# Optimization experiments

Measured on AMD Instinct MI355X. Metric: run time of the kernel, lower is better.

Reference implementation:

```python
import jax, jax.numpy as jnp
import numpy as np
from jax import lax

B = 1
D, H, W = 16, 16, 32
L = D * H * W
C = 96          # hidden_dim
DIN = 96        # d_inner = expansion_factor(1) * hidden_dim
N = 16          # d_state
R = 6           # dt_rank = ceil(C / 16)
K = 8           # scan directions: 4 axis orders x {fwd, bwd}
PERMS = [(0, 1, 2), (1, 2, 0), (2, 0, 1), (2, 1, 0)]


def _ln(x, w, b, eps):
    m = x.mean(-1, keepdims=True)
    v = ((x - m) ** 2).mean(-1, keepdims=True)
    return (x - m) * lax.rsqrt(v + eps) * w + b


def _conv3d(x, w, b, groups=1):
    y = lax.conv_general_dilated(x, w, (1, 1, 1), 'SAME', feature_group_count=groups,
                                 dimension_numbers=('NCDHW', 'OIDHW', 'NCDHW'))
    return y + b[None, :, None, None, None]


def _ss3d(x5, in_proj_w, conv_w, conv_b, x_proj_w, dt_w, dt_b, A_logs, Ds,
          out_norm_w, out_norm_b, out_proj_w):
    b, d, h, w, _ = x5.shape
    l = d * h * w
    spatial = (d, h, w)
    xz = jnp.einsum('bdhwc,ec->bdhwe', x5, in_proj_w)          # (b,d,h,w,2*DIN)
    x, z = jnp.split(xz, 2, axis=-1)
    x = jnp.transpose(x, (0, 4, 1, 2, 3))                       # (b,DIN,d,h,w)
    x = jax.nn.silu(_conv3d(x, conv_w, conv_b, groups=DIN))     # depthwise conv
    # build K/2 axis-order scans, then add reversed copies -> K directions
    xs = jnp.stack([jnp.transpose(x, (0, 1, 2 + p[0], 2 + p[1], 2 + p[2])).reshape(b, DIN, l)
                    for p in PERMS], axis=1)                    # (b,4,DIN,l)
    xs = jnp.concatenate([xs, jnp.flip(xs, -1)], axis=1)        # (b,K,DIN,l)
    x_dbl = jnp.einsum('bkdl,ked->bkel', xs, x_proj_w)          # e = R+2N
    dts, Bs, Cs = x_dbl[:, :, :R], x_dbl[:, :, R:R + N], x_dbl[:, :, R + N:]
    dts = jax.nn.softplus(jnp.einsum('bkrl,kdr->bkdl', dts, dt_w) + dt_b[None, :, :, None])
    A = -jnp.exp(A_logs)                                        # (K,DIN,N)
    # time-major for the selective scan
    dts_t = jnp.moveaxis(dts, -1, 0)                            # (l,b,K,DIN)
    xs_t = jnp.moveaxis(xs, -1, 0)
    Bs_t = jnp.moveaxis(Bs, -1, 0)                              # (l,b,K,N)
    Cs_t = jnp.moveaxis(Cs, -1, 0)

    def step(hc, inps):
        dt, u, Bt, Ct = inps
        hc = jnp.exp(dt[..., None] * A) * hc + (dt * u)[..., None] * Bt[:, :, None, :]
        y = jnp.einsum('bkdn,bkn->bkd', hc, Ct)
        return hc, y

    h0 = jnp.zeros((b, K, DIN, N), x.dtype)
    _, ys = lax.scan(step, h0, (dts_t, xs_t, Bs_t, Cs_t))       # ys: (l,b,K,DIN)
    ys = jnp.moveaxis(ys, 0, -1) + Ds[None, :, :, None] * xs    # (b,K,DIN,l)
    y_f, y_b = ys[:, :4], jnp.flip(ys[:, 4:], -1)
    acc = jnp.zeros((b, DIN, l), x.dtype)
    for i, p in enumerate(PERMS):
        inv = np.argsort(p)
        pshape = tuple(spatial[ax] for ax in p)
        for yk in (y_f[:, i], y_b[:, i]):
            yk = yk.reshape(b, DIN, *pshape)
            yk = jnp.transpose(yk, (0, 1, 2 + int(inv[0]), 2 + int(inv[1]), 2 + int(inv[2])))
            acc = acc + yk.reshape(b, DIN, l)
    y = _ln(jnp.transpose(acc, (0, 2, 1)), out_norm_w, out_norm_b, 1e-5)
    y = y.reshape(b, d, h, w, DIN) * jax.nn.silu(z)
    return jnp.einsum('bdhwe,ce->bdhwc', y, out_proj_w)


def _cab(x, cab_w1, cab_b1, cab_w2, cab_b2, ca_w1, ca_b1, ca_w2, ca_b2):
    # x: (b,C,d,h,w); conv -> GELU -> conv -> channel attention
    t = jax.nn.gelu(_conv3d(x, cab_w1, cab_b1), approximate=False)
    t = _conv3d(t, cab_w2, cab_b2)
    m = t.mean(axis=(2, 3, 4))                                  # global avg pool (b,C)
    v = jax.nn.relu(m @ ca_w1.T + ca_b1)
    v = jax.nn.sigmoid(v @ ca_w2.T + ca_b2)
    return t * v[:, :, None, None, None]


def _forward(inp, ln1_w, ln1_b, skip1, skip2, ln2_w, ln2_b, in_proj_w, conv_w, conv_b,
             x_proj_w, dt_w, dt_b, A_logs, Ds, out_norm_w, out_norm_b, out_proj_w,
             cab_w1, cab_b1, cab_w2, cab_b2, ca_w1, ca_b1, ca_w2, ca_b2, x_size):
    b, l, c = inp.shape
    d, h, w = x_size
    x5 = inp.reshape(b, d, h, w, c)
    xn = _ln(x5, ln1_w, ln1_b, 1e-6)
    attn = _ss3d(xn, in_proj_w, conv_w, conv_b, x_proj_w, dt_w, dt_b, A_logs, Ds,
                 out_norm_w, out_norm_b, out_proj_w)
    x = x5 * skip1 + attn                                       # drop_path = identity (rate 0)
    y2 = jnp.transpose(_ln(x, ln2_w, ln2_b, 1e-5), (0, 4, 1, 2, 3))
    cab = _cab(y2, cab_w1, cab_b1, cab_w2, cab_b2, ca_w1, ca_b1, ca_w2, ca_b2)
    x = x * skip2 + jnp.transpose(cab, (0, 2, 3, 4, 1))
    return x.reshape(b, l, c)


def setup_inputs() -> dict:
    key = jax.random.key(0)
    ks = jax.random.split(key, 12)
    g = lambda i, shp, s=0.02: jax.random.normal(ks[i], shp, jnp.float32) * s
    return {
        'inp': jax.random.normal(ks[0], (B, L, C), jnp.float32),
        'x_size': (D, H, W),
        'ln1_w': jnp.ones((C,), jnp.float32), 'ln1_b': jnp.zeros((C,), jnp.float32),
        'skip1': jnp.ones((C,), jnp.float32), 'skip2': jnp.ones((C,), jnp.float32),
        'ln2_w': jnp.ones((C,), jnp.float32), 'ln2_b': jnp.zeros((C,), jnp.float32),
        'in_proj_w': g(1, (2 * DIN, C)),
        'conv_w': g(2, (DIN, 1, 3, 3, 3), 0.1), 'conv_b': jnp.zeros((DIN,), jnp.float32),
        'x_proj_w': g(3, (K, R + 2 * N, DIN)),
        'dt_w': g(4, (K, DIN, R), 0.1), 'dt_b': g(5, (K, DIN), 0.1),
        'A_logs': jnp.log(jnp.tile(jnp.arange(1, N + 1, dtype=jnp.float32), (K, DIN, 1))),
        'Ds': jnp.ones((K, DIN), jnp.float32),
        'out_norm_w': jnp.ones((DIN,), jnp.float32), 'out_norm_b': jnp.zeros((DIN,), jnp.float32),
        'out_proj_w': g(6, (C, DIN)),
        'cab_w1': g(7, (C // 3, C, 3, 3, 3), 0.05), 'cab_b1': jnp.zeros((C // 3,), jnp.float32),
        'cab_w2': g(8, (C, C // 3, 3, 3, 3), 0.05), 'cab_b2': jnp.zeros((C,), jnp.float32),
        'ca_w1': g(9, (C // 2, C)), 'ca_b1': jnp.zeros((C // 2,), jnp.float32),
        'ca_w2': g(10, (C, C // 2)), 'ca_b2': jnp.zeros((C,), jnp.float32),
    }


def reference(inp, ln1_w, ln1_b, skip1, skip2, ln2_w, ln2_b, in_proj_w, conv_w, conv_b,
              x_proj_w, dt_w, dt_b, A_logs, Ds, out_norm_w, out_norm_b, out_proj_w,
              cab_w1, cab_b1, cab_w2, cab_b2, ca_w1, ca_b1, ca_w2, ca_b2, x_size):
    return _forward(inp, ln1_w, ln1_b, skip1, skip2, ln2_w, ln2_b, in_proj_w, conv_w, conv_b,
                    x_proj_w, dt_w, dt_b, A_logs, Ds, out_norm_w, out_norm_b, out_proj_w,
                    cab_w1, cab_b1, cab_w2, cab_b2, ca_w1, ca_b1, ca_w2, ca_b2, x_size)
```

## Files before the change

kernel.cpp:

```cpp
#include <hip/hip_runtime.h>
#include <math.h>

#define LL 8192
#define CC 96
#define DINc 96
#define NN 16
#define RR 6
#define KK 8
#define Dd 16
#define Hh 16
#define Ww 32
#define NCH 32
#define CHL 256

__constant__ int Pc_[4][3] = {{0,1,2},{1,2,0},{2,0,1},{2,1,0}};

__device__ __forceinline__ float silu_(float x){ return x / (1.f + __expf(-x)); }

__global__ void k_ln1(const float* __restrict__ inp, const float* __restrict__ w,
                      const float* __restrict__ b, float* __restrict__ xn_cm) {
    __shared__ float tile[16][97];
    __shared__ float smean[16], srstd[16];
    int l0 = blockIdx.x * 16;
    int tid = threadIdx.x;
    #pragma unroll
    for (int r = 0; r < 6; ++r) {
        int e = r * 256 + tid;
        int lo = e / 96, c = e % 96;
        tile[lo][c] = inp[(long)(l0 + lo) * 96 + c];
    }
    __syncthreads();
    {
        int lo = tid >> 4, g = tid & 15;
        float ps = 0.f;
        #pragma unroll
        for (int j = 0; j < 6; ++j) ps += tile[lo][g * 6 + j];
        #pragma unroll
        for (int o = 1; o < 16; o <<= 1) ps += __shfl_xor(ps, o, 16);
        float m = ps * (1.f / 96.f);
        float pv = 0.f;
        #pragma unroll
        for (int j = 0; j < 6; ++j) { float dd = tile[lo][g * 6 + j] - m; pv += dd * dd; }
        #pragma unroll
        for (int o = 1; o < 16; o <<= 1) pv += __shfl_xor(pv, o, 16);
        if (g == 0) { smean[lo] = m; srstd[lo] = rsqrtf(pv * (1.f / 96.f) + 1e-6f); }
    }
    __syncthreads();
    #pragma unroll
    for (int r = 0; r < 6; ++r) {
        int e = r * 256 + tid;
        int c = e >> 4, lo = e & 15;
        xn_cm[(long)c * LL + l0 + lo] = (tile[lo][c] - smean[lo]) * srstd[lo] * w[c] + b[c];
    }
}

__global__ void k_wtrans(const float* __restrict__ inpj, const float* __restrict__ xpw,
                         const float* __restrict__ w1, const float* __restrict__ w2,
                         const float* __restrict__ opw,
                         float* __restrict__ ipT, float* __restrict__ xpT,
                         float* __restrict__ wT1, float* __restrict__ wT2,
                         float* __restrict__ opT) {
    int idx = blockIdx.x * blockDim.x + threadIdx.x;
    if (idx < 82944) {
        int oc = idx & 31; int tap = (idx >> 5) % 27; int ic = idx / (32 * 27);
        wT1[idx] = w1[(oc * 96 + ic) * 27 + tap];
    }
    if (idx < 82944) {
        int oc = idx % 96; int tap = (idx / 96) % 27; int ic = idx / (96 * 27);
        wT2[idx] = w2[(oc * 32 + ic) * 27 + tap];
    }
    if (idx < 18432) {
        int e = idx % 192; int c = idx / 192;
        ipT[idx] = inpj[e * 96 + c];
    }
    if (idx < 29184) {
        int e = idx % 38; int c = (idx / 38) % 96; int k = idx / (38 * 96);
        xpT[idx] = xpw[(k * 38 + e) * 96 + c];
    }
    if (idx < 9216) {
        int c = idx % 96; int e = idx / 96;
        opT[idx] = opw[c * 96 + e];
    }
}

__global__ void k_inproj(const float* __restrict__ xn_cm, const float* __restrict__ ipT,
                         float* __restrict__ xcm, float* __restrict__ z_rm) {
    int bx = blockIdx.x;
    int eb = bx >> 5;
    int l  = ((bx & 31) << 8) + threadIdx.x;
    int e0 = eb << 3;
    float a[8];
    #pragma unroll
    for (int j = 0; j < 8; ++j) a[j] = 0.f;
    const float* wp = ipT + e0;
    for (int c = 0; c < CC; ++c) {
        float x = xn_cm[c * LL + l];
        const float4* wv = (const float4*)(wp + c * 192);
        float4 wa = wv[0], wb = wv[1];
        a[0] += x * wa.x; a[1] += x * wa.y; a[2] += x * wa.z; a[3] += x * wa.w;
        a[4] += x * wb.x; a[5] += x * wb.y; a[6] += x * wb.z; a[7] += x * wb.w;
    }
    if (e0 < DINc) {
        float* dst = xcm + (long)e0 * LL;
        #pragma unroll
        for (int j = 0; j < 8; ++j) dst[(long)j * LL + l] = a[j];
    } else {
        float* dst = z_rm + (long)l * DINc + (e0 - DINc);
        #pragma unroll
        for (int j = 0; j < 8; ++j) dst[j] = a[j];
    }
}

__global__ void k_dwconv(const float* __restrict__ xcm, const float* __restrict__ cw,
                         const float* __restrict__ cb, float* __restrict__ xs0) {
    int bx = blockIdx.x;
    int c  = bx >> 3;
    int l4 = ((bx & 7) << 8) + threadIdx.x;
    int w0 = (l4 & 7) << 2;
    int h  = (l4 >> 3) & 15;
    int d  = l4 >> 7;
    int l  = (d * Hh + h) * Ww + w0;
    float wk[27];
    #pragma unroll
    for (int t = 0; t < 27; ++t) wk[t] = cw[c * 27 + t];
    float rmask[9]; int roff[9];
    #pragma unroll
    for (int kd = 0; kd < 3; ++kd) {
        int dd = d + kd - 1;
        bool vd = (unsigned)dd < Dd; int dc = vd ? dd : 0;
        #pragma unroll
        for (int kh = 0; kh < 3; ++kh) {
            int hh = h + kh - 1;
            bool vh = (unsigned)hh < Hh; int hcl = vh ? hh : 0;
            rmask[kd * 3 + kh] = (vd && vh) ? 1.f : 0.f;
            roff[kd * 3 + kh]  = (dc * Hh + hcl) * Ww + w0;
        }
    }
    float mleft  = (w0 > 0)  ? 1.f : 0.f;
    float mright = (w0 < 28) ? 1.f : 0.f;
    float a0 = cb[c], a1 = a0, a2 = a0, a3 = a0;
    const float* xp = xcm + (long)c * LL;
    #pragma unroll
    for (int r = 0; r < 9; ++r) {
        float rm = rmask[r];
        const float* xr = xp + roff[r];
        float4 xc = *(const float4*)xr;
        float v[6];
        v[0] = xr[-1] * (rm * mleft);
        v[1] = xc.x * rm; v[2] = xc.y * rm; v[3] = xc.z * rm; v[4] = xc.w * rm;
        v[5] = xr[4] * (rm * mright);
        #pragma unroll
        for (int t = 0; t < 3; ++t) {
            float wv = wk[r * 3 + t];
            a0 += v[t + 0] * wv;
            a1 += v[t + 1] * wv;
            a2 += v[t + 2] * wv;
            a3 += v[t + 3] * wv;
        }
    }
    *(float4*)(xs0 + (long)c * LL + l) = make_float4(silu_(a0), silu_(a1), silu_(a2), silu_(a3));
}

__global__ void k_permA(float* __restrict__ xs) {
    __shared__ float lv[8192 + 256 + 16];
    int bx = blockIdx.x;
    int k = bx / 96 + 1;
    int c = bx % 96;
    const float* src = xs + (long)c * LL;
    float* dst = xs + ((long)k * DINc + c) * LL;
    int tid = threadIdx.x;
    for (int i = tid; i < LL; i += 256)
        lv[i + (i >> 5) + (i >> 9)] = src[i];
    __syncthreads();
    int p0 = Pc_[k][0], p1 = Pc_[k][1], p2 = Pc_[k][2];
    const int sp[3] = {Dd, Hh, Ww};
    int pd1 = sp[p1], pd2 = sp[p2];
    for (int i = tid; i < LL; i += 256) {
        int i2 = i % pd2;
        int t  = i / pd2;
        int i1 = t % pd1;
        int i0 = t / pd1;
        int coord[3];
        coord[p0] = i0; coord[p1] = i1; coord[p2] = i2;
        int o = (coord[0] * Hh + coord[1]) * Ww + coord[2];
        dst[i] = lv[o + (o >> 5) + (o >> 9)];
    }
}

__global__ void k_permB(float* __restrict__ xs) {
    int idx = blockIdx.x * blockDim.x + threadIdx.x;
    if (idx >= 4 * DINc * (LL / 4)) return;
    int q = idx & (LL / 4 - 1);
    int c = (idx >> 11) % DINc;
    int k = idx / (DINc * (LL / 4));
    const float4* src = (const float4*)(xs + ((long)k * DINc + c) * LL);
    float4 s = src[LL / 4 - 1 - q];
    float4* dst = (float4*)(xs + ((long)(k + 4) * DINc + c) * LL);
    dst[q] = make_float4(s.w, s.z, s.y, s.x);
}

__global__ void k_xdbl(const float* __restrict__ xs, const float* __restrict__ xpT,
                       float* __restrict__ dtr, float* __restrict__ Bb, float* __restrict__ Cb) {
    int bx = blockIdx.x;
    int k = bx >> 6;
    int rest = bx & 63;
    int eh = rest & 1;
    int lblk = rest >> 1;
    int l = (lblk << 8) + threadIdx.x;
    int e0 = eh * 19;
    float acc[19];
    #pragma unroll
    for (int e = 0; e < 19; ++e) acc[e] = 0.f;
    const float* xb = xs + (long)k * DINc * LL + l;
    const float* wb = xpT + k * DINc * 38 + e0;
    for (int c = 0; c < DINc; ++c) {
        float x = xb[(long)c * LL];
        const float* wr = wb + c * 38;
        #pragma unroll
        for (int e = 0; e < 19; ++e) acc[e] += x * wr[e];
    }
    int lq = l >> 2, q = l & 3;
    #pragma unroll
    for (int e = 0; e < 19; ++e) {
        int ge = e0 + e;
        if (ge < RR)
            dtr[((long)k * LL + l) * 6 + ge] = acc[e];
        else if (ge < RR + NN)
            Bb[(((long)k * 2048 + lq) * 16 + (ge - RR)) * 4 + q] = acc[e];
        else
            Cb[(((long)k * 2048 + lq) * 16 + (ge - RR - NN)) * 4 + q] = acc[e];
    }
}

__device__ __forceinline__ float softplus_(float x) {
    return (x > 20.f) ? x : __logf(1.f + __expf(x));
}

__global__ __launch_bounds__(512)
void k_scanf(float* __restrict__ xs_ys, const float* __restrict__ dtr,
             const float* __restrict__ Bb, const float* __restrict__ Cb,
             const float* __restrict__ A_logs, const float* __restrict__ dt_w,
             const float* __restrict__ dt_b, const float* __restrict__ Ds) {
    __shared__ __align__(16) float sdt[LL + (LL >> 7) * 4];
    __shared__ float sAp[16][33];
    __shared__ float sBc[16][33];
    __shared__ float shs[16][33];
    int bx = blockIdx.x;
    int grp = (bx & 7) * DINc + (bx >> 3);
    int k = grp / DINc;
    int tid = threadIdx.x;
    int n = tid & 15;
    int chunk = tid >> 4;
    {
        float w0 = dt_w[grp * RR + 0], w1 = dt_w[grp * RR + 1], w2 = dt_w[grp * RR + 2];
        float w3 = dt_w[grp * RR + 3], w4 = dt_w[grp * RR + 4], w5 = dt_w[grp * RR + 5];
        float dtb = dt_b[grp];
        const float* drb = dtr + (long)k * LL * 6;
        for (int i = tid; i < LL; i += 512) {
            const float2* dp = (const float2*)(drb + (long)i * 6);
            float2 d0 = dp[0], d1 = dp[1], d2 = dp[2];
            float dtl = dtb + d0.x * w0 + d0.y * w1 + d1.x * w2 + d1.y * w3 + d2.x * w4 + d2.y * w5;
            sdt[i + ((i >> 7) << 2)] = softplus_(dtl);
        }
    }
    __syncthreads();
    float A_n = -__expf(A_logs[grp * NN + n]);
    const float4* sdt4 = (const float4*)sdt;
    int dbase = chunk * 66;
    const float4* u4 = (const float4*)(xs_ys + (long)grp * LL + chunk * CHL);
    const float4* B4 = (const float4*)Bb + ((long)k * 2048 + chunk * (CHL / 4)) * 16 + n;
    const float4* C4 = (const float4*)Cb + ((long)k * 2048 + chunk * (CHL / 4)) * 16 + n;
    {
        float hc = 0.f, dsum = 0.f;
        #pragma unroll 4
        for (int q = 0; q < CHL / 4; ++q) {
            float4 dt = sdt4[dbase + q + (q >> 5)];
            float4 uu = u4[q];
            float4 Bv = B4[q * 16];
            dsum += (dt.x + dt.y) + (dt.z + dt.w);
            hc = __expf(dt.x * A_n) * hc + (dt.x * uu.x) * Bv.x;
            hc = __expf(dt.y * A_n) * hc + (dt.y * uu.y) * Bv.y;
            hc = __expf(dt.z * A_n) * hc + (dt.z * uu.z) * Bv.z;
            hc = __expf(dt.w * A_n) * hc + (dt.w * uu.w) * Bv.w;
        }
        sAp[n][chunk] = __expf(A_n * dsum);
        sBc[n][chunk] = hc;
    }
    __syncthreads();
    if (tid < 16) {
        float h = 0.f;
        for (int c = 0; c < NCH; ++c) {
            shs[tid][c] = h;
            h = sAp[tid][c] * h + sBc[tid][c];
        }
    }
    __syncthreads();
    float Dv = Ds[grp];
    float* urow = xs_ys + (long)grp * LL + chunk * CHL;
    float hc = shs[n][chunk];
    int qsel = n >> 2, csel = n & 3;
    bool b0 = (n & 1), b1 = ((n >> 1) & 1), b2 = ((n >> 2) & 1), b3 = (n >> 3);
    for (int base = 0; base < CHL; base += 16) {
        float u_lane = 0.f;
        float p[16];
        #pragma unroll
        for (int q = 0; q < 4; ++q) {
            int qq = (base >> 2) + q;
            float4 dt = sdt4[dbase + qq + (qq >> 5)];
            float4 uu = *(const float4*)(urow + base + q * 4);
            float4 Bv = B4[qq * 16];
            float4 Cv = C4[qq * 16];
            if (q == qsel)
                u_lane = (csel == 0) ? uu.x : (csel == 1) ? uu.y : (csel == 2) ? uu.z : uu.w;
            hc = __expf(dt.x * A_n) * hc + (dt.x * uu.x) * Bv.x;  p[q*4+0] = hc * Cv.x;
            hc = __expf(dt.y * A_n) * hc + (dt.y * uu.y) * Bv.y;  p[q*4+1] = hc * Cv.y;
            hc = __expf(dt.z * A_n) * hc + (dt.z * uu.z) * Bv.z;  p[q*4+2] = hc * Cv.z;
            hc = __expf(dt.w * A_n) * hc + (dt.w * uu.w) * Bv.w;  p[q*4+3] = hc * Cv.w;
        }
        float q8[8];
        #pragma unroll
        for (int m = 0; m < 8; ++m) {
            float sel = b0 ? p[2*m] : p[2*m+1];
            float r = __shfl_xor(sel, 1, 16);
            q8[m] = (b0 ? p[2*m+1] : p[2*m]) + r;
        }
        float r4[4];
        #pragma unroll
        for (int m = 0; m < 4; ++m) {
            float sel = b1 ? q8[2*m] : q8[2*m+1];
            float r = __shfl_xor(sel, 2, 16);
            r4[m] = (b1 ? q8[2*m+1] : q8[2*m]) + r;
        }
        float t2r[2];
        #pragma unroll
        for (int m = 0; m < 2; ++m) {
            float sel = b2 ? r4[2*m] : r4[2*m+1];
            float r = __shfl_xor(sel, 4, 16);
            t2r[m] = (b2 ? r4[2*m+1] : r4[2*m]) + r;
        }
        float sel = b3 ? t2r[0] : t2r[1];
        float r = __shfl_xor(sel, 8, 16);
        float yv = (b3 ? t2r[1] : t2r[0]) + r;
        urow[base + n] = yv + Dv * u_lane;
    }
}

__global__ void k_combproj(const float* __restrict__ ys, const float* __restrict__ z_rm,
                           const float* __restrict__ w, const float* __restrict__ b,
                           const float* __restrict__ opT, const float* __restrict__ inp,
                           const float* __restrict__ skip1, float* __restrict__ xafter) {
    __shared__ float sy[4][96];
    int wave = threadIdx.x >> 6;
    int lane = threadIdx.x & 63;
    int l = blockIdx.x * 4 + wave;
    int d = l >> 9, h = (l >> 5) & 15, wd = l & 31;
    int lps[4];
    lps[0] = l;
    lps[1] = (h * 32 + wd) * 16 + d;
    lps[2] = (wd * 16 + d) * 16 + h;
    lps[3] = (wd * 16 + h) * 16 + d;
    int c0 = lane, c1 = 64 + lane;
    float a0 = 0.f, a1 = 0.f;
    #pragma unroll
    for (int i = 0; i < 4; ++i) {
        a0 += ys[((long)(i * 96) + c0) * LL + lps[i]];
        a0 += ys[((long)((4 + i) * 96) + c0) * LL + (LL - 1 - lps[i])];
    }
    if (lane < 32) {
        #pragma unroll
        for (int i = 0; i < 4; ++i) {
            a1 += ys[((long)(i * 96) + c1) * LL + lps[i]];
            a1 += ys[((long)((4 + i) * 96) + c1) * LL + (LL - 1 - lps[i])];
        }
    }
    float s = a0 + a1;
    #pragma unroll
    for (int o = 1; o < 64; o <<= 1) s += __shfl_xor(s, o, 64);
    float m = s * (1.f / 96.f);
    float d0 = a0 - m;
    float d1 = (lane < 32) ? (a1 - m) : 0.f;
    float ss = d0 * d0 + d1 * d1;
    #pragma unroll
    for (int o = 1; o < 64; o <<= 1) ss += __shfl_xor(ss, o, 64);
    float r = rsqrtf(ss * (1.f / 96.f) + 1e-5f);
    float zz = z_rm[(long)l * 96 + c0];
    sy[wave][c0] = (d0 * r * w[c0] + b[c0]) * silu_(zz);
    if (lane < 32) {
        float z1 = z_rm[(long)l * 96 + c1];
        sy[wave][c1] = (d1 * r * w[c1] + b[c1]) * silu_(z1);
    }
    __syncthreads();
    int c1g = (lane < 32) ? c1 : 0;
    float o0 = 0.f, o1 = 0.f;
    #pragma unroll 4
    for (int e = 0; e < 96; ++e) {
        float ye = sy[wave][e];
        o0 += ye * opT[e * 96 + c0];
        o1 += ye * opT[e * 96 + c1g];
    }
    xafter[(long)l * 96 + c0] = inp[(long)l * 96 + c0] * skip1[c0] + o0;
    if (lane < 32)
        xafter[(long)l * 96 + c1] = inp[(long)l * 96 + c1] * skip1[c1] + o1;
}

__global__ void k_ln2(const float* __restrict__ xafter, const float* __restrict__ w,
                      const float* __restrict__ b, float* __restrict__ y2) {
    __shared__ float tile[16][97];
    __shared__ float smean[16], srstd[16];
    int l0 = blockIdx.x * 16;
    int tid = threadIdx.x;
    #pragma unroll
    for (int r = 0; r < 6; ++r) {
        int e = r * 256 + tid;
        int lo = e / 96, c = e % 96;
        tile[lo][c] = xafter[(long)(l0 + lo) * 96 + c];
    }
    __syncthreads();
    {
        int lo = tid >> 4, g = tid & 15;
        float ps = 0.f;
        #pragma unroll
        for (int j = 0; j < 6; ++j) ps += tile[lo][g * 6 + j];
        #pragma unroll
        for (int o = 1; o < 16; o <<= 1) ps += __shfl_xor(ps, o, 16);
        float m = ps * (1.f / 96.f);
        float pv = 0.f;
        #pragma unroll
        for (int j = 0; j < 6; ++j) { float dd = tile[lo][g * 6 + j] - m; pv += dd * dd; }
        #pragma unroll
        for (int o = 1; o < 16; o <<= 1) pv += __shfl_xor(pv, o, 16);
        if (g == 0) { smean[lo] = m; srstd[lo] = rsqrtf(pv * (1.f / 96.f) + 1e-5f); }
    }
    __syncthreads();
    #pragma unroll
    for (int r = 0; r < 6; ++r) {
        int e = r * 256 + tid;
        int c = e >> 4, lo = e & 15;
        y2[(long)c * LL + l0 + lo] = (tile[lo][c] - smean[lo]) * srstd[lo] * w[c] + b[c];
    }
}

__global__ void k_conv1(const float* __restrict__ y2, const float* __restrict__ wT,
                        float* __restrict__ part) {
    int bx = blockIdx.x;
    int g  = bx >> 3;
    int ocg = g & 7;
    int isp = g >> 3;
    int l4 = ((bx & 7) << 8) + threadIdx.x;
    int w0 = (l4 & 7) << 2;
    int h  = (l4 >> 3) & 15;
    int d  = l4 >> 7;
    int l  = (d * Hh + h) * Ww + w0;
    float rmask[9]; int roff[9];
    #pragma unroll
    for (int kd = 0; kd < 3; ++kd) {
        int dd = d + kd - 1;
        bool vd = (unsigned)dd < Dd; int dc = vd ? dd : 0;
        #pragma unroll
        for (int kh = 0; kh < 3; ++kh) {
            int hh = h + kh - 1;
            bool vh = (unsigned)hh < Hh; int hcl = vh ? hh : 0;
            rmask[kd * 3 + kh] = (vd && vh) ? 1.f : 0.f;
            roff[kd * 3 + kh]  = (dc * Hh + hcl) * Ww + w0;
        }
    }
    float mleft  = (w0 > 0)  ? 1.f : 0.f;
    float mright = (w0 < 28) ? 1.f : 0.f;
    float acc[16];
    #pragma unroll
    for (int j = 0; j < 16; ++j) acc[j] = 0.f;
    for (int ic = isp * 6; ic < isp * 6 + 6; ++ic) {
        const float* xp = y2 + (long)ic * LL;
        const float* wb = wT + ic * 864 + ocg * 4;
        #pragma unroll
        for (int r = 0; r < 9; ++r) {
            float rm = rmask[r];
            const float* xr = xp + roff[r];
            float4 xc = *(const float4*)xr;
            float v[6];
            v[0] = xr[-1] * (rm * mleft);
            v[1] = xc.x * rm; v[2] = xc.y * rm; v[3] = xc.z * rm; v[4] = xc.w * rm;
            v[5] = xr[4] * (rm * mright);
            #pragma unroll
            for (int t = 0; t < 3; ++t) {
                float4 wa = *(const float4*)(wb + (r * 3 + t) * 32);
                #pragma unroll
                for (int p = 0; p < 4; ++p) {
                    float x = v[t + p];
                    acc[0  + p] += x * wa.x;  acc[4  + p] += x * wa.y;
                    acc[8  + p] += x * wa.z;  acc[12 + p] += x * wa.w;
                }
            }
        }
    }
    float* pp = part + ((long)(isp * 32 + ocg * 4)) * LL + l;
    #pragma unroll
    for (int oc = 0; oc < 4; ++oc)
        *(float4*)(pp + (long)oc * LL) = make_float4(acc[oc*4+0], acc[oc*4+1], acc[oc*4+2], acc[oc*4+3]);
}

__global__ void k_gelusum(const float* __restrict__ part, const float* __restrict__ b1,
                          float* __restrict__ t1) {
    int idx = blockIdx.x * blockDim.x + threadIdx.x;
    if (idx >= 32 * LL) return;
    int l = idx & (LL - 1);
    int oc = idx >> 13;
    float s = b1[oc];
    #pragma unroll
    for (int isp = 0; isp < 16; ++isp)
        s += part[((long)(isp * 32 + oc)) * LL + l];
    t1[oc * LL + l] = 0.5f * s * (1.f + erff(s * 0.70710678118654752f));
}

__global__ void k_conv2(const float* __restrict__ t1, const float* __restrict__ wT,
                        float* __restrict__ part) {
    int bx = blockIdx.x;
    int g  = bx >> 3;
    int ocg = g % 24;
    int isp = g / 24;
    int l4 = ((bx & 7) << 8) + threadIdx.x;
    int w0 = (l4 & 7) << 2;
    int h  = (l4 >> 3) & 15;
    int d  = l4 >> 7;
    int l  = (d * Hh + h) * Ww + w0;
    float rmask[9]; int roff[9];
    #pragma unroll
    for (int kd = 0; kd < 3; ++kd) {
        int dd = d + kd - 1;
        bool vd = (unsigned)dd < Dd; int dc = vd ? dd : 0;
        #pragma unroll
        for (int kh = 0; kh < 3; ++kh) {
            int hh = h + kh - 1;
            bool vh = (unsigned)hh < Hh; int hcl = vh ? hh : 0;
            rmask[kd * 3 + kh] = (vd && vh) ? 1.f : 0.f;
            roff[kd * 3 + kh]  = (dc * Hh + hcl) * Ww + w0;
        }
    }
    float mleft  = (w0 > 0)  ? 1.f : 0.f;
    float mright = (w0 < 28) ? 1.f : 0.f;
    float acc[16];
    #pragma unroll
    for (int j = 0; j < 16; ++j) acc[j] = 0.f;
    for (int ic = isp * 4; ic < isp * 4 + 4; ++ic) {
        const float* xp = t1 + (long)ic * LL;
        const float* wb = wT + ic * 2592 + ocg * 4;
        #pragma unroll
        for (int r = 0; r < 9; ++r) {
            float rm = rmask[r];
            const float* xr = xp + roff[r];
            float4 xc = *(const float4*)xr;
            float v[6];
            v[0] = xr[-1] * (rm * mleft);
            v[1] = xc.x * rm; v[2] = xc.y * rm; v[3] = xc.z * rm; v[4] = xc.w * rm;
            v[5] = xr[4] * (rm * mright);
            #pragma unroll
            for (int t = 0; t < 3; ++t) {
                float4 wa = *(const float4*)(wb + (r * 3 + t) * 96);
                #pragma unroll
                for (int p = 0; p < 4; ++p) {
                    float x = v[t + p];
                    acc[0  + p] += x * wa.x;  acc[4  + p] += x * wa.y;
                    acc[8  + p] += x * wa.z;  acc[12 + p] += x * wa.w;
                }
            }
        }
    }
    float* pp = part + ((long)(isp * 96 + ocg * 4)) * LL + l;
    #pragma unroll
    for (int oc = 0; oc < 4; ++oc)
        *(float4*)(pp + (long)oc * LL) = make_float4(acc[oc*4+0], acc[oc*4+1], acc[oc*4+2], acc[oc*4+3]);
}

__global__ void k_conv2sum(const float* __restrict__ part, const float* __restrict__ b2,
                           float* __restrict__ t2) {
    int idx = blockIdx.x * blockDim.x + threadIdx.x;
    if (idx >= 96 * LL) return;
    int l = idx & (LL - 1);
    int oc = idx >> 13;
    float s = b2[oc];
    #pragma unroll
    for (int isp = 0; isp < 8; ++isp)
        s += part[((long)(isp * 96 + oc)) * LL + l];
    t2[oc * LL + l] = s;
}

__global__ void k_mean(const float* __restrict__ t2, float* __restrict__ mbuf) {
    __shared__ float sm[256];
    int c = blockIdx.x;
    const float4* tp = (const float4*)(t2 + (long)c * LL);
    float a = 0.f;
    for (int q = threadIdx.x; q < LL / 4; q += 256) {
        float4 v = tp[q];
        a += (v.x + v.y) + (v.z + v.w);
    }
    sm[threadIdx.x] = a;
    __syncthreads();
    for (int o = 128; o > 0; o >>= 1) {
        if (threadIdx.x < o) sm[threadIdx.x] += sm[threadIdx.x + o];
        __syncthreads();
    }
    if (threadIdx.x == 0) mbuf[c] = sm[0] * (1.f / LL);
}

__global__ void k_mlp(const float* __restrict__ mbuf, const float* __restrict__ w1,
                      const float* __restrict__ b1, const float* __restrict__ w2,
                      const float* __restrict__ b2, float* __restrict__ v2) {
    __shared__ float v[48];
    int t = threadIdx.x;
    if (t < 48) {
        float s = b1[t];
        for (int c = 0; c < 96; ++c) s += mbuf[c] * w1[t * 96 + c];
        v[t] = fmaxf(s, 0.f);
    }
    __syncthreads();
    if (t < 96) {
        float s = b2[t];
        for (int j = 0; j < 48; ++j) s += v[j] * w2[t * 48 + j];
        v2[t] = 1.f / (1.f + __expf(-s));
    }
}

__global__ void k_final(const float* __restrict__ xafter, const float* __restrict__ skip2,
                        const float* __restrict__ t2, const float* __restrict__ v2,
                        float* __restrict__ out) {
    __shared__ float tile[96][17];
    __shared__ float sk2[96], sv2[96];
    int l0 = blockIdx.x * 16;
    int tid = threadIdx.x;
    if (tid < 96) { sk2[tid] = skip2[tid]; sv2[tid] = v2[tid]; }
    #pragma unroll
    for (int r = 0; r < 6; ++r) {
        int e = r * 256 + tid;
        int c = e >> 4, lo = e & 15;
        tile[c][lo] = t2[(long)c * LL + l0 + lo];
    }
    __syncthreads();
    #pragma unroll
    for (int r = 0; r < 6; ++r) {
        int e = r * 256 + tid;
        int lo = e / 96, c = e % 96;
        long gi = (long)(l0 + lo) * 96 + c;
        out[gi] = xafter[gi] * sk2[c] + tile[c][lo] * sv2[c];
    }
}

static const size_t OFF_XS     = 0;
static const size_t OFF_Z      = 6291456;
static const size_t OFF_XCM    = 7077888;
static const size_t OFF_XN     = 7864320;
static const size_t OFF_DTRAW  = 8650752;
static const size_t OFF_BB     = 9043968;
static const size_t OFF_CB     = 10092544;
static const size_t OFF_XAFTER = 11141120;
static const size_t OFF_Y2     = 11927552;
static const size_t OFF_T1     = 12713984;
static const size_t OFF_T2     = 12976128;
static const size_t OFF_MV     = 13762560;
static const size_t OFF_WT1    = 13762816;
static const size_t OFF_WT2    = 13845760;
static const size_t OFF_IPT    = 13928704;
static const size_t OFF_XPT    = 13947136;
static const size_t OFF_OPT    = 13976320;

extern "C" void kernel_launch(void* const* d_in, const int* in_sizes, int n_in,
                              void* d_out, int out_size, void* d_ws, size_t ws_size,
                              hipStream_t stream) {
    const float* inp    = (const float*)d_in[0];
    const float* ln1_w  = (const float*)d_in[2];
    const float* ln1_b  = (const float*)d_in[3];
    const float* skip1  = (const float*)d_in[4];
    const float* skip2  = (const float*)d_in[5];
    const float* ln2_w  = (const float*)d_in[6];
    const float* ln2_b  = (const float*)d_in[7];
    const float* inpj   = (const float*)d_in[8];
    const float* conv_w = (const float*)d_in[9];
    const float* conv_b = (const float*)d_in[10];
    const float* xpw    = (const float*)d_in[11];
    const float* dt_w   = (const float*)d_in[12];
    const float* dt_b   = (const float*)d_in[13];
    const float* A_logs = (const float*)d_in[14];
    const float* Ds     = (const float*)d_in[15];
    const float* onw    = (const float*)d_in[16];
    const float* onb    = (const float*)d_in[17];
    const float* opw    = (const float*)d_in[18];
    const float* cab_w1 = (const float*)d_in[19];
    const float* cab_b1 = (const float*)d_in[20];
    const float* cab_w2 = (const float*)d_in[21];
    const float* cab_b2 = (const float*)d_in[22];
    const float* ca_w1  = (const float*)d_in[23];
    const float* ca_b1  = (const float*)d_in[24];
    const float* ca_w2  = (const float*)d_in[25];
    const float* ca_b2  = (const float*)d_in[26];

    float* ws = (float*)d_ws;
    float* xs     = ws + OFF_XS;
    float* zbuf   = ws + OFF_Z;
    float* xcm    = ws + OFF_XCM;
    float* xn     = ws + OFF_XN;
    float* dtr    = ws + OFF_DTRAW;
    float* Bb     = ws + OFF_BB;
    float* Cb     = ws + OFF_CB;
    float* xafter = ws + OFF_XAFTER;
    float* y2     = ws + OFF_Y2;
    float* t1     = ws + OFF_T1;
    float* t2     = ws + OFF_T2;
    float* mv     = ws + OFF_MV;
    float* wT1    = ws + OFF_WT1;
    float* wT2    = ws + OFF_WT2;
    float* ipT    = ws + OFF_IPT;
    float* xpT    = ws + OFF_XPT;
    float* opT    = ws + OFF_OPT;
    float* part1  = xs;
    float* part2  = xs;

    float* out = (float*)d_out;
    #define GRID(n) dim3((unsigned)(((n) + 255) / 256)), dim3(256)

    hipLaunchKernelGGL(k_ln1,     dim3(512), dim3(256),       0, stream, inp, ln1_w, ln1_b, xn);
    hipLaunchKernelGGL(k_wtrans,  GRID(82944),                0, stream, inpj, xpw, cab_w1, cab_w2, opw, ipT, xpT, wT1, wT2, opT);
    hipLaunchKernelGGL(k_inproj,  dim3(768), dim3(256),       0, stream, xn, ipT, xcm, zbuf);
    hipLaunchKernelGGL(k_dwconv,  dim3(768), dim3(256),       0, stream, xcm, conv_w, conv_b, xs);
    hipLaunchKernelGGL(k_permA,   dim3(288), dim3(256),       0, stream, xs);
    hipLaunchKernelGGL(k_permB,   GRID(4 * DINc * (LL / 4)),  0, stream, xs);
    hipLaunchKernelGGL(k_xdbl,    dim3(512), dim3(256),       0, stream, xs, xpT, dtr, Bb, Cb);
    hipLaunchKernelGGL(k_scanf,   dim3(KK * DINc), dim3(512), 0, stream, xs, dtr, Bb, Cb, A_logs, dt_w, dt_b, Ds);
    hipLaunchKernelGGL(k_combproj,dim3(LL / 4), dim3(256),    0, stream, xs, zbuf, onw, onb, opT, inp, skip1, xafter);
    hipLaunchKernelGGL(k_ln2,     dim3(512), dim3(256),       0, stream, xafter, ln2_w, ln2_b, y2);
    hipLaunchKernelGGL(k_conv1,   dim3(1024), dim3(256),      0, stream, y2, wT1, part1);
    hipLaunchKernelGGL(k_gelusum, GRID(32 * LL),              0, stream, part1, cab_b1, t1);
    hipLaunchKernelGGL(k_conv2,   dim3(1536), dim3(256),      0, stream, t1, wT2, part2);
    hipLaunchKernelGGL(k_conv2sum,GRID(96 * LL),              0, stream, part2, cab_b2, t2);
    hipLaunchKernelGGL(k_mean,    dim3(96), dim3(256),        0, stream, t2, mv);
    hipLaunchKernelGGL(k_mlp,     dim3(1), dim3(128),         0, stream, mv, ca_w1, ca_b1, ca_w2, ca_b2, mv + 96);
    hipLaunchKernelGGL(k_final,   dim3(512), dim3(256),       0, stream, xafter, skip2, t2, mv + 96, out);
    #undef GRID
}
```

Baseline: 277.1 us.

## Fuse reversed-direction copies into producers, use exp2 in scan, vectorize partial sums

The reversed scan directions are now written directly by the depthwise conv and permute kernels, so the separate k_permB pass that re-read and re-wrote half of xs goes away. The selective scan folds log2(e) into A and calls the hardware exp2 builtin instead of __expf. The two partial-sum reduction kernels (gelusum, conv2sum) now process four elements per thread with float4 loads and stores. The extra writes in k_permA are reversed-order scalar stores, which may coalesce less well.

```diff
diff --git a/kernel.cpp b/kernel.cpp
--- a/kernel.cpp
+++ b/kernel.cpp
@@ -12,6 +12,9 @@
 #define Ww 32
 #define NCH 32
 #define CHL 256
+#define LOG2E 1.44269504088896340736f
+
+__device__ __forceinline__ float ex2_(float x) { return __builtin_amdgcn_exp2f(x); }
 
 __constant__ int Pc_[4][3] = {{0,1,2},{1,2,0},{2,0,1},{2,1,0}};
 
@@ -112,7 +115,7 @@
 }
 
 __global__ void k_dwconv(const float* __restrict__ xcm, const float* __restrict__ cw,
-                         const float* __restrict__ cb, float* __restrict__ xs0) {
+                         const float* __restrict__ cb, float* __restrict__ xs) {
     int bx = blockIdx.x;
     int c  = bx >> 3;
     int l4 = ((bx & 7) << 8) + threadIdx.x;
@@ -158,7 +161,9 @@
             a3 += v[t + 3] * wv;
         }
     }
-    *(float4*)(xs0 + (long)c * LL + l) = make_float4(silu_(a0), silu_(a1), silu_(a2), silu_(a3));
+    float s0 = silu_(a0), s1 = silu_(a1), s2 = silu_(a2), s3 = silu_(a3);
+    *(float4*)(xs + (long)c * LL + l) = make_float4(s0, s1, s2, s3);
+    *(float4*)(xs + ((long)(4 * DINc) + c) * LL + (LL - 4 - l)) = make_float4(s3, s2, s1, s0);
 }
 
 __global__ void k_permA(float* __restrict__ xs) {
@@ -167,7 +172,8 @@
     int k = bx / 96 + 1;
     int c = bx % 96;
     const float* src = xs + (long)c * LL;
-    float* dst = xs + ((long)k * DINc + c) * LL;
+    float* dst  = xs + ((long)k * DINc + c) * LL;
+    float* dst4 = xs + ((long)(k + 4) * DINc + c) * LL;
     int tid = threadIdx.x;
     for (int i = tid; i < LL; i += 256)
         lv[i + (i >> 5) + (i >> 9)] = src[i];
@@ -183,20 +189,10 @@
         int coord[3];
         coord[p0] = i0; coord[p1] = i1; coord[p2] = i2;
         int o = (coord[0] * Hh + coord[1]) * Ww + coord[2];
-        dst[i] = lv[o + (o >> 5) + (o >> 9)];
-    }
-}
-
-__global__ void k_permB(float* __restrict__ xs) {
-    int idx = blockIdx.x * blockDim.x + threadIdx.x;
-    if (idx >= 4 * DINc * (LL / 4)) return;
-    int q = idx & (LL / 4 - 1);
-    int c = (idx >> 11) % DINc;
-    int k = idx / (DINc * (LL / 4));
-    const float4* src = (const float4*)(xs + ((long)k * DINc + c) * LL);
-    float4 s = src[LL / 4 - 1 - q];
-    float4* dst = (float4*)(xs + ((long)(k + 4) * DINc + c) * LL);
-    dst[q] = make_float4(s.w, s.z, s.y, s.x);
+        float v = lv[o + (o >> 5) + (o >> 9)];
+        dst[i] = v;
+        dst4[LL - 1 - i] = v;
+    }
 }
 
 __global__ void k_xdbl(const float* __restrict__ xs, const float* __restrict__ xpT,
@@ -264,7 +260,7 @@
         }
     }
     __syncthreads();
-    float A_n = -__expf(A_logs[grp * NN + n]);
+    float A2 = -__expf(A_logs[grp * NN + n]) * LOG2E;
     const float4* sdt4 = (const float4*)sdt;
     int dbase = chunk * 66;
     const float4* u4 = (const float4*)(xs_ys + (long)grp * LL + chunk * CHL);
@@ -278,12 +274,12 @@
             float4 uu = u4[q];
             float4 Bv = B4[q * 16];
             dsum += (dt.x + dt.y) + (dt.z + dt.w);
-            hc = __expf(dt.x * A_n) * hc + (dt.x * uu.x) * Bv.x;
-            hc = __expf(dt.y * A_n) * hc + (dt.y * uu.y) * Bv.y;
-            hc = __expf(dt.z * A_n) * hc + (dt.z * uu.z) * Bv.z;
-            hc = __expf(dt.w * A_n) * hc + (dt.w * uu.w) * Bv.w;
-        }
-        sAp[n][chunk] = __expf(A_n * dsum);
+            hc = ex2_(dt.x * A2) * hc + (dt.x * uu.x) * Bv.x;
+            hc = ex2_(dt.y * A2) * hc + (dt.y * uu.y) * Bv.y;
+            hc = ex2_(dt.z * A2) * hc + (dt.z * uu.z) * Bv.z;
+            hc = ex2_(dt.w * A2) * hc + (dt.w * uu.w) * Bv.w;
+        }
+        sAp[n][chunk] = ex2_(A2 * dsum);
         sBc[n][chunk] = hc;
     }
     __syncthreads();
@@ -312,10 +308,10 @@
             float4 Cv = C4[qq * 16];
             if (q == qsel)
                 u_lane = (csel == 0) ? uu.x : (csel == 1) ? uu.y : (csel == 2) ? uu.z : uu.w;
-            hc = __expf(dt.x * A_n) * hc + (dt.x * uu.x) * Bv.x;  p[q*4+0] = hc * Cv.x;
-            hc = __expf(dt.y * A_n) * hc + (dt.y * uu.y) * Bv.y;  p[q*4+1] = hc * Cv.y;
-            hc = __expf(dt.z * A_n) * hc + (dt.z * uu.z) * Bv.z;  p[q*4+2] = hc * Cv.z;
-            hc = __expf(dt.w * A_n) * hc + (dt.w * uu.w) * Bv.w;  p[q*4+3] = hc * Cv.w;
+            hc = ex2_(dt.x * A2) * hc + (dt.x * uu.x) * Bv.x;  p[q*4+0] = hc * Cv.x;
+            hc = ex2_(dt.y * A2) * hc + (dt.y * uu.y) * Bv.y;  p[q*4+1] = hc * Cv.y;
+            hc = ex2_(dt.z * A2) * hc + (dt.z * uu.z) * Bv.z;  p[q*4+2] = hc * Cv.z;
+            hc = ex2_(dt.w * A2) * hc + (dt.w * uu.w) * Bv.w;  p[q*4+3] = hc * Cv.w;
         }
         float q8[8];
         #pragma unroll
@@ -502,14 +498,22 @@
 __global__ void k_gelusum(const float* __restrict__ part, const float* __restrict__ b1,
                           float* __restrict__ t1) {
     int idx = blockIdx.x * blockDim.x + threadIdx.x;
-    if (idx >= 32 * LL) return;
-    int l = idx & (LL - 1);
-    int oc = idx >> 13;
-    float s = b1[oc];
-    #pragma unroll
-    for (int isp = 0; isp < 16; ++isp)
-        s += part[((long)(isp * 32 + oc)) * LL + l];
-    t1[oc * LL + l] = 0.5f * s * (1.f + erff(s * 0.70710678118654752f));
+    if (idx >= 32 * (LL / 4)) return;
+    int lq = idx & (LL / 4 - 1);
+    int oc = idx >> 11;
+    float bv = b1[oc];
+    float4 s = make_float4(bv, bv, bv, bv);
+    #pragma unroll
+    for (int isp = 0; isp < 16; ++isp) {
+        float4 v = *(const float4*)(part + ((long)(isp * 32 + oc)) * LL + lq * 4);
+        s.x += v.x; s.y += v.y; s.z += v.z; s.w += v.w;
+    }
+    float4 o;
+    o.x = 0.5f * s.x * (1.f + erff(s.x * 0.70710678118654752f));
+    o.y = 0.5f * s.y * (1.f + erff(s.y * 0.70710678118654752f));
+    o.z = 0.5f * s.z * (1.f + erff(s.z * 0.70710678118654752f));
+    o.w = 0.5f * s.w * (1.f + erff(s.w * 0.70710678118654752f));
+    *(float4*)(t1 + (long)oc * LL + lq * 4) = o;
 }
 
 __global__ void k_conv2(const float* __restrict__ t1, const float* __restrict__ wT,
@@ -574,14 +578,17 @@
 __global__ void k_conv2sum(const float* __restrict__ part, const float* __restrict__ b2,
                            float* __restrict__ t2) {
     int idx = blockIdx.x * blockDim.x + threadIdx.x;
-    if (idx >= 96 * LL) return;
-    int l = idx & (LL - 1);
-    int oc = idx >> 13;
-    float s = b2[oc];
-    #pragma unroll
-    for (int isp = 0; isp < 8; ++isp)
-        s += part[((long)(isp * 96 + oc)) * LL + l];
-    t2[oc * LL + l] = s;
+    if (idx >= 96 * (LL / 4)) return;
+    int lq = idx & (LL / 4 - 1);
+    int oc = idx >> 11;
+    float bv = b2[oc];
+    float4 s = make_float4(bv, bv, bv, bv);
+    #pragma unroll
+    for (int isp = 0; isp < 8; ++isp) {
+        float4 v = *(const float4*)(part + ((long)(isp * 96 + oc)) * LL + lq * 4);
+        s.x += v.x; s.y += v.y; s.z += v.z; s.w += v.w;
+    }
+    *(float4*)(t2 + (long)oc * LL + lq * 4) = s;
 }
 
 __global__ void k_mean(const float* __restrict__ t2, float* __restrict__ mbuf) {
@@ -721,15 +728,14 @@
     hipLaunchKernelGGL(k_inproj,  dim3(768), dim3(256),       0, stream, xn, ipT, xcm, zbuf);
     hipLaunchKernelGGL(k_dwconv,  dim3(768), dim3(256),       0, stream, xcm, conv_w, conv_b, xs);
     hipLaunchKernelGGL(k_permA,   dim3(288), dim3(256),       0, stream, xs);
-    hipLaunchKernelGGL(k_permB,   GRID(4 * DINc * (LL / 4)),  0, stream, xs);
     hipLaunchKernelGGL(k_xdbl,    dim3(512), dim3(256),       0, stream, xs, xpT, dtr, Bb, Cb);
     hipLaunchKernelGGL(k_scanf,   dim3(KK * DINc), dim3(512), 0, stream, xs, dtr, Bb, Cb, A_logs, dt_w, dt_b, Ds);
     hipLaunchKernelGGL(k_combproj,dim3(LL / 4), dim3(256),    0, stream, xs, zbuf, onw, onb, opT, inp, skip1, xafter);
     hipLaunchKernelGGL(k_ln2,     dim3(512), dim3(256),       0, stream, xafter, ln2_w, ln2_b, y2);
     hipLaunchKernelGGL(k_conv1,   dim3(1024), dim3(256),      0, stream, y2, wT1, part1);
-    hipLaunchKernelGGL(k_gelusum, GRID(32 * LL),              0, stream, part1, cab_b1, t1);
+    hipLaunchKernelGGL(k_gelusum, GRID(32 * (LL / 4)),        0, stream, part1, cab_b1, t1);
     hipLaunchKernelGGL(k_conv2,   dim3(1536), dim3(256),      0, stream, t1, wT2, part2);
-    hipLaunchKernelGGL(k_conv2sum,GRID(96 * LL),              0, stream, part2, cab_b2, t2);
+    hipLaunchKernelGGL(k_conv2sum,GRID(96 * (LL / 4)),        0, stream, part2, cab_b2, t2);
     hipLaunchKernelGGL(k_mean,    dim3(96), dim3(256),        0, stream, t2, mv);
     hipLaunchKernelGGL(k_mlp,     dim3(1), dim3(128),         0, stream, mv, ca_w1, ca_b1, ca_w2, ca_b2, mv + 96);
     hipLaunchKernelGGL(k_final,   dim3(512), dim3(256),       0, stream, xafter, skip2, t2, mv + 96, out);
```

New measurement: 270.2 us. -2.5%, faster.
